# Kernel tuning notes

Measured on AMD Instinct MI355X. Metric: run time of the kernel, lower is better.

The kernel has to match this reference:

```python
import jax, jax.numpy as jnp
import numpy as np

B, L, F, U, P, CAT = 64, 25, 128, 10000, 10000, 400
PI = 3.141592653589793


def haversine(lat1, lon1, lat2, lon2):
    p = PI / 180.0
    a = 0.5 - jnp.cos((lat2 - lat1) * p) / 2 \
        + jnp.cos(lat1 * p) * jnp.cos(lat2 * p) * (1 - jnp.cos((lon2 - lon1) * p)) / 2
    return 12742.0 * jnp.arcsin(jnp.sqrt(a))


def setup_inputs() -> dict:
    key = jax.random.key(0)
    ks = jax.random.split(key, 24)
    s = 0.02
    return {
        "user": jax.random.randint(ks[0], (B, L), 0, U),
        "poi": jax.random.randint(ks[1], (B, L), 0, P),
        "cat": jax.random.randint(ks[2], (B, L), 0, CAT),
        "lat": jax.random.uniform(ks[3], (B, L), dtype=jnp.float32),
        "lon": jax.random.uniform(ks[4], (B, L), dtype=jnp.float32),
        "tod": jax.random.randint(ks[5], (B, L), 0, 24),
        "dow": jax.random.randint(ks[6], (B, L), 0, 7),
        "unixtime": jax.random.uniform(ks[7], (B, L), dtype=jnp.float32),
        "user_emb_w": jax.random.normal(ks[8], (U, F), jnp.float32) * s,
        "poi_emb_w": jax.random.normal(ks[9], (P, F), jnp.float32) * s,
        "tod_emb_w": jax.random.normal(ks[10], (24, F), jnp.float32) * s,
        "dow_emb_w": jax.random.normal(ks[11], (7, F), jnp.float32) * s,
        "Wq": jax.random.normal(ks[12], (F, F), jnp.float32) * s,
        "bq": jnp.zeros((F,), jnp.float32),
        "Wk": jax.random.normal(ks[13], (F, F), jnp.float32) * s,
        "bk": jnp.zeros((F,), jnp.float32),
        "Wv": jax.random.normal(ks[14], (F, F), jnp.float32) * s,
        "bv": jnp.zeros((F,), jnp.float32),
        "w_val": jax.random.normal(ks[15], (L,), jnp.float32) * 0.2,
        "b_val": jnp.zeros((), jnp.float32),
        "distance_matrix": jax.random.uniform(ks[16], (P, P), dtype=jnp.float32),
    }


def reference(user, poi, cat, lat, lon, tod, dow, unixtime,
              user_emb_w, poi_emb_w, tod_emb_w, dow_emb_w,
              Wq, bq, Wk, bk, Wv, bv, w_val, b_val, distance_matrix):
    # token embeddings  [B,L,F]
    inputs = user_emb_w[user] + poi_emb_w[poi] + tod_emb_w[tod] + dow_emb_w[dow]

    # pairwise haversine / time deltas  [B,L,L]  (vectorized double loop)
    delta_s = haversine(lat[:, :, None], lon[:, :, None], lat[:, None, :], lon[:, None, :])
    delta_t = jnp.abs(unixtime[:, :, None] - unixtime[:, None, :])
    su, sl = delta_s.max(), delta_s.min()
    tu, tl = delta_t.max(), delta_t.min()
    delta = (jnp.exp(-delta_s / (su - sl)) + jnp.exp(-delta_t / (tu - tl))) / 2

    # successive time intervals  [B,L], first column = 0
    time_interval = jnp.concatenate(
        [jnp.zeros((B, 1), unixtime.dtype), jnp.abs(unixtime[:, 1:] - unixtime[:, :-1])], axis=1)
    interval_s = distance_matrix[poi]            # [B,L,P] gather of candidate distances
    interval_t = time_interval[:, :, None]       # broadcast to [B,L,P]
    su1, sl1 = interval_s.max(), interval_s.min()
    tu1, tl1 = time_interval.max(), time_interval.min()
    interval = (jnp.exp(-interval_s / (su1 - sl1)) + jnp.exp(-interval_t / (tu1 - tl1))) / 2

    # additive-bias self-attention
    q = inputs @ Wq + bq
    k = inputs @ Wk + bk
    v = inputs @ Wv + bv
    scores = jnp.einsum('bif,bjf->bij', q, k) + delta
    attn_w = jax.nn.softmax(scores, axis=-1)
    self_attn_out = jnp.einsum('bij,bjf->bif', attn_w, v)   # [B,L,F]

    # candidate attention over all POIs, weighted by spatio-temporal interval
    cand_attn = jnp.einsum('pf,blf->bpl', poi_emb_w, self_attn_out) \
        * jnp.swapaxes(interval, 1, 2)                      # [B,P,L]
    pre = cand_attn @ w_val + b_val                          # Linear(25,1) -> [B,P]
    return (pre, pre)
```

## Files before the change

### kernel.cpp

```cpp
#include <hip/hip_runtime.h>
#include <math.h>

#define BB 64
#define LL 25
#define FF 128
#define PP 10000

#define OFF_RED 0
#define OFF_TT  16
#define OFF_C1  1616
#define OFF_C2  3216
#define OFF_DS  4816
#define OFF_DT  44816
#define OFF_Q   84816
#define OFF_K   289616
#define OFF_V   494416
#define OFF_AH  699216
#define OFF_AL  830288
#define OFF_BH  961360
#define OFF_BL  1608528

#define NEG_INF -3.402823466e38f
#define POS_INF  3.402823466e38f

typedef short bf16x8 __attribute__((ext_vector_type(8)));
typedef float f32x16 __attribute__((ext_vector_type(16)));

__device__ inline unsigned short f2bf(float x) {
    unsigned u = __float_as_uint(x);
    u += 0x7FFFu + ((u >> 16) & 1u);
    return (unsigned short)(u >> 16);
}
__device__ inline float bf2f(unsigned short h) {
    return __uint_as_float(((unsigned)h) << 16);
}

template <bool MAX>
__device__ float blockReduce(float v) {
    __shared__ float sh[8];
    const int lane = threadIdx.x & 63;
    const int wid  = threadIdx.x >> 6;
#pragma unroll
    for (int off = 32; off > 0; off >>= 1) {
        float o = __shfl_down(v, off, 64);
        v = MAX ? fmaxf(v, o) : fminf(v, o);
    }
    __syncthreads();
    if (lane == 0) sh[wid] = v;
    __syncthreads();
    if (threadIdx.x == 0) {
        const int nw = blockDim.x >> 6;
        for (int w = 1; w < nw; ++w) v = MAX ? fmaxf(v, sh[w]) : fminf(v, sh[w]);
    }
    return v;
}

__global__ void k_prep(const float* __restrict__ pe, float* __restrict__ ws) {
    const int gid = blockIdx.x * 256 + threadIdx.x;
    if (gid < 8) ((int*)ws)[gid] = (gid & 1) ? 0x7F800000 : (int)0xFF800000u;
    if (gid >= PP * FF) return;
    const int p = gid >> 7, f = gid & 127;
    const float x = pe[gid];
    const unsigned short h = f2bf(x);
    const unsigned short l = f2bf(x - bf2f(h));
    const int c = p >> 5, n = p & 31, kk = f >> 4, kh = (f >> 3) & 1, j = f & 7;
    const int pos = ((c * 8 + kk) * 64 + (kh * 32 + n)) * 8 + j;
    ((unsigned short*)(ws + OFF_BH))[pos] = h;
    ((unsigned short*)(ws + OFF_BL))[pos] = l;
}

__global__ void k_geo(const float* __restrict__ lat, const float* __restrict__ lon,
                      const float* __restrict__ ut, float* __restrict__ ws) {
    const int b = blockIdx.x, t = threadIdx.x;
    __shared__ float la[LL], lo[LL], uu[LL];
    if (t < LL) { la[t] = lat[b * LL + t]; lo[t] = lon[b * LL + t]; uu[t] = ut[b * LL + t]; }
    __syncthreads();
    float dsmax = NEG_INF, dsmin = POS_INF, dtmax = NEG_INF, dtmin = POS_INF;
    const float p = 0.017453292519943295f;
    for (int idx = t; idx < LL * LL; idx += 256) {
        int i = idx / LL, j = idx % LL;
        float a = 0.5f - cosf((la[j] - la[i]) * p) * 0.5f
                + cosf(la[i] * p) * cosf(la[j] * p) * (1.0f - cosf((lo[j] - lo[i]) * p)) * 0.5f;
        float d  = 12742.0f * asinf(sqrtf(a));
        float dt = fabsf(uu[i] - uu[j]);
        ws[OFF_DS + b * 625 + idx] = d;
        ws[OFF_DT + b * 625 + idx] = dt;
        dsmax = fmaxf(dsmax, d); dsmin = fminf(dsmin, d);
        dtmax = fmaxf(dtmax, dt); dtmin = fminf(dtmin, dt);
    }
    int* red = (int*)ws;
    float r;
    r = blockReduce<true >(dsmax); if (!t) atomicMax(&red[0], __float_as_int(r));
    r = blockReduce<false>(dsmin); if (!t) atomicMin(&red[1], __float_as_int(r));
    r = blockReduce<true >(dtmax); if (!t) atomicMax(&red[2], __float_as_int(r));
    r = blockReduce<false>(dtmin); if (!t) atomicMin(&red[3], __float_as_int(r));
    float ttv = 0.0f;
    if (t < LL) {
        ttv = (t == 0) ? 0.0f : fabsf(uu[t] - uu[t - 1]);
        ws[OFF_TT + b * LL + t] = ttv;
    }
    float tmax = (t < LL) ? ttv : NEG_INF;
    float tmin = (t < LL) ? ttv : POS_INF;
    r = blockReduce<true >(tmax); if (!t) atomicMax(&red[6], __float_as_int(r));
    r = blockReduce<false>(tmin); if (!t) atomicMin(&red[7], __float_as_int(r));
}

__global__ void k_qkv(const int* __restrict__ user, const int* __restrict__ poi,
                      const int* __restrict__ tod, const int* __restrict__ dow,
                      const float* __restrict__ ue, const float* __restrict__ pe,
                      const float* __restrict__ te, const float* __restrict__ de,
                      const float* __restrict__ Wq, const float* __restrict__ bq,
                      const float* __restrict__ Wk, const float* __restrict__ bk,
                      const float* __restrict__ Wv, const float* __restrict__ bv,
                      float* __restrict__ ws) {
    const int b = blockIdx.x, m = blockIdx.y, t = threadIdx.x;
    __shared__ __align__(16) float xs[26 * FF];
    __shared__ int ids[4][LL];
    if (t < LL) {
        ids[0][t] = user[b * LL + t]; ids[1][t] = poi[b * LL + t];
        ids[2][t] = tod[b * LL + t];  ids[3][t] = dow[b * LL + t];
    }
    if (t < FF) xs[LL * FF + t] = 0.0f;
    __syncthreads();
    for (int idx = t; idx < LL * FF; idx += 256) {
        int l = idx >> 7, f = idx & 127;
        xs[idx] = ue[ids[0][l] * FF + f] + pe[ids[1][l] * FF + f]
                + te[ids[2][l] * FF + f] + de[ids[3][l] * FF + f];
    }
    __syncthreads();
    const float* W    = (m == 0) ? Wq : (m == 1) ? Wk : Wv;
    const float* bias = (m == 0) ? bq : (m == 1) ? bk : bv;
    float* o = ws + ((m == 0) ? OFF_Q : (m == 1) ? OFF_K : OFF_V) + b * LL * FF;
    const int f  = t & 127;
    const int l0 = (t >> 7) * 13;
    float acc[13];
#pragma unroll
    for (int i = 0; i < 13; ++i) acc[i] = 0.0f;
    for (int g = 0; g < FF; g += 4) {
        float w0 = W[(g + 0) * FF + f];
        float w1 = W[(g + 1) * FF + f];
        float w2 = W[(g + 2) * FF + f];
        float w3 = W[(g + 3) * FF + f];
#pragma unroll
        for (int i = 0; i < 13; ++i) {
            float4 x = *(const float4*)(xs + (l0 + i) * FF + g);
            acc[i] = fmaf(x.w, w3, fmaf(x.z, w2, fmaf(x.y, w1, fmaf(x.x, w0, acc[i]))));
        }
    }
    float bb = bias[f];
#pragma unroll
    for (int i = 0; i < 13; ++i) {
        int l = l0 + i;
        if (l < LL) o[l * FF + f] = acc[i] + bb;
    }
}

__global__ void k_rowred(const int* __restrict__ poi, const float* __restrict__ dm,
                         float* __restrict__ ws) {
    const int t = threadIdx.x;
    float mx = NEG_INF, mn = POS_INF;
#pragma unroll
    for (int rr = 0; rr < 4; ++rr) {
        const int r = poi[blockIdx.x * 4 + rr];
        const float4* row = (const float4*)(dm + (size_t)r * PP);
        for (int i = t; i < PP / 4; i += 256) {
            float4 v = row[i];
            mx = fmaxf(mx, fmaxf(fmaxf(v.x, v.y), fmaxf(v.z, v.w)));
            mn = fminf(mn, fminf(fminf(v.x, v.y), fminf(v.z, v.w)));
        }
    }
    int* red = (int*)ws;
    float rr2;
    rr2 = blockReduce<true >(mx); if (!t) atomicMax(&red[4], __float_as_int(rr2));
    rr2 = blockReduce<false>(mn); if (!t) atomicMin(&red[5], __float_as_int(rr2));
}

__global__ void k_attn(const float* __restrict__ w_val, float* __restrict__ ws) {
    const int b = blockIdx.x, t = threadIdx.x;
    __shared__ float qs[LL * 129], ks[LL * 129], vs[LL * FF], sc[LL * LL];
    const int* red = (const int*)ws;
    const float su  = __int_as_float(red[0]), sl  = __int_as_float(red[1]);
    const float tu  = __int_as_float(red[2]), tl  = __int_as_float(red[3]);
    const float tu1 = __int_as_float(red[6]), tl1 = __int_as_float(red[7]);
    const float nS0 = -1.0f / (su - sl), nT0 = -1.0f / (tu - tl), nT1 = -1.0f / (tu1 - tl1);
    for (int idx = t; idx < LL * FF; idx += 256) {
        int l = idx >> 7, f = idx & 127;
        qs[l * 129 + f] = ws[OFF_Q + b * LL * FF + idx];
        ks[l * 129 + f] = ws[OFF_K + b * LL * FF + idx];
        vs[idx]         = ws[OFF_V + b * LL * FF + idx];
    }
    __syncthreads();
    for (int idx = t; idx < LL * LL; idx += 256) {
        int i = idx / LL, j = idx % LL;
        float a = 0.0f;
        for (int f = 0; f < FF; ++f) a = fmaf(qs[i * 129 + f], ks[j * 129 + f], a);
        float d  = ws[OFF_DS + b * 625 + idx];
        float dt = ws[OFF_DT + b * 625 + idx];
        sc[idx] = a + 0.5f * (expf(d * nS0) + expf(dt * nT0));
    }
    __syncthreads();
    if (t < LL) {
        float m = NEG_INF;
        for (int j = 0; j < LL; ++j) m = fmaxf(m, sc[t * LL + j]);
        float s = 0.0f;
        for (int j = 0; j < LL; ++j) { float e = expf(sc[t * LL + j] - m); sc[t * LL + j] = e; s += e; }
        float inv = 1.0f / s;
        for (int j = 0; j < LL; ++j) sc[t * LL + j] *= inv;
    }
    __syncthreads();
    unsigned short* Ah = (unsigned short*)(ws + OFF_AH);
    unsigned short* Al = (unsigned short*)(ws + OFF_AL);
    for (int idx = t; idx < LL * FF; idx += 256) {
        int l = idx >> 7, f = idx & 127;
        float a = 0.0f;
        for (int j = 0; j < LL; ++j) a = fmaf(sc[l * LL + j], vs[j * FF + f], a);
        unsigned short h  = f2bf(a);
        unsigned short lo = f2bf(a - bf2f(h));
        int kk = f >> 4, kh = (f >> 3) & 1, j = f & 7;
        int pos = ((b * 8 + kk) * 64 + (kh * 32 + l)) * 8 + j;
        Ah[pos] = h; Al[pos] = lo;
    }
    if (t < LL) {
        float ttv = ws[OFF_TT + b * LL + t];
        float wv  = w_val[t];
        ws[OFF_C1 + b * LL + t] = 0.5f * wv * expf(ttv * nT1);
        ws[OFF_C2 + b * LL + t] = 0.5f * wv;
    }
}

__global__ void __launch_bounds__(256) k_main(const int* __restrict__ poi,
                                              const float* __restrict__ dm,
                                              const float* __restrict__ bval_p,
                                              const float* __restrict__ ws,
                                              float* __restrict__ out) {
    const int t = threadIdx.x;
    const int wave = t >> 6, lane = t & 63;
    const int half = lane >> 5, col = lane & 31;
    __shared__ float lc1[BB * 32], lc2[BB * 32];
    __shared__ int   lrw[BB * 32];
    for (int idx = t; idx < BB * LL; idx += 256) {
        int b = idx / LL, l = idx - b * LL;
        lc1[b * 32 + l] = ws[OFF_C1 + idx];
        lc2[b * 32 + l] = ws[OFF_C2 + idx];
        lrw[b * 32 + l] = poi[idx];
    }
    __syncthreads();
    const int* red = (const int*)ws;
    const float su1 = __int_as_float(red[4]), sl1 = __int_as_float(red[5]);
    const float nS1 = -1.0f / (su1 - sl1);
    const float bv  = bval_p[0];
    const int ct  = blockIdx.x * 4 + wave;
    const int p   = ct * 32 + col;
    const int pcl = min(p, PP - 1);
    const bf16x8* Bh = (const bf16x8*)(ws + OFF_BH);
    const bf16x8* Bl = (const bf16x8*)(ws + OFF_BL);
    const bf16x8* Ah = (const bf16x8*)(ws + OFF_AH);
    const bf16x8* Al = (const bf16x8*)(ws + OFF_AL);
    bf16x8 bh[8], bl[8];
#pragma unroll
    for (int kk = 0; kk < 8; ++kk) {
        bh[kk] = Bh[(ct * 8 + kk) * 64 + lane];
        bl[kk] = Bl[(ct * 8 + kk) * 64 + lane];
    }
    const int b0 = blockIdx.y * 8;
    for (int bi = 0; bi < 8; ++bi) {
        const int b = b0 + bi;
        f32x16 acc = {};
#pragma unroll
        for (int kk = 0; kk < 8; ++kk) {
            bf16x8 ah = Ah[(b * 8 + kk) * 64 + lane];
            bf16x8 al = Al[(b * 8 + kk) * 64 + lane];
            acc = __builtin_amdgcn_mfma_f32_32x32x16_bf16(ah, bh[kk], acc, 0, 0, 0);
            acc = __builtin_amdgcn_mfma_f32_32x32x16_bf16(al, bh[kk], acc, 0, 0, 0);
            acc = __builtin_amdgcn_mfma_f32_32x32x16_bf16(ah, bl[kk], acc, 0, 0, 0);
        }
        float sum = 0.0f;
#pragma unroll
        for (int r = 0; r < 16; ++r) {
            int row  = (r & 3) + 8 * (r >> 2) + 4 * half;
            int rowc = min(row, LL - 1);
            float d  = dm[(size_t)lrw[b * 32 + rowc] * PP + pcl];
            float w  = lc1[b * 32 + rowc] + lc2[b * 32 + rowc] * expf(d * nS1);
            w = (row < LL) ? w : 0.0f;
            sum = fmaf(w, acc[r], sum);
        }
        sum += __shfl_xor(sum, 32, 64);
        sum += bv;
        if (half == 0 && p < PP) {
            out[b * PP + p]           = sum;
            out[BB * PP + b * PP + p] = sum;
        }
    }
}

extern "C" void kernel_launch(void* const* d_in, const int* in_sizes, int n_in,
                              void* d_out, int out_size, void* d_ws, size_t ws_size,
                              hipStream_t stream) {
    const int*   user = (const int*)d_in[0];
    const int*   poi  = (const int*)d_in[1];
    const float* lat  = (const float*)d_in[3];
    const float* lon  = (const float*)d_in[4];
    const int*   tod  = (const int*)d_in[5];
    const int*   dow  = (const int*)d_in[6];
    const float* ut   = (const float*)d_in[7];
    const float* ue   = (const float*)d_in[8];
    const float* pe   = (const float*)d_in[9];
    const float* te   = (const float*)d_in[10];
    const float* de   = (const float*)d_in[11];
    const float* Wq   = (const float*)d_in[12];
    const float* bq   = (const float*)d_in[13];
    const float* Wk   = (const float*)d_in[14];
    const float* bk   = (const float*)d_in[15];
    const float* Wv   = (const float*)d_in[16];
    const float* bv   = (const float*)d_in[17];
    const float* w_val = (const float*)d_in[18];
    const float* b_val = (const float*)d_in[19];
    const float* dm   = (const float*)d_in[20];
    float* out = (float*)d_out;
    float* ws  = (float*)d_ws;

    k_prep<<<(PP * FF + 255) / 256, 256, 0, stream>>>(pe, ws);
    k_geo<<<BB, 256, 0, stream>>>(lat, lon, ut, ws);
    k_qkv<<<dim3(BB, 3), 256, 0, stream>>>(user, poi, tod, dow, ue, pe, te, de,
                                           Wq, bq, Wk, bk, Wv, bv, ws);
    k_rowred<<<(BB * LL) / 4, 256, 0, stream>>>(poi, dm, ws);
    k_attn<<<BB, 256, 0, stream>>>(w_val, ws);
    k_main<<<dim3(79, 8), 256, 0, stream>>>(poi, dm, b_val, ws, out);
}
```

Measured before the change: 605.4 us.

## Merge front-end kernels into one launch and replace atomics with partial reductions

Fuses the prep, geo, QKV and distance-row reduction kernels into a single launch that dispatches on block index, removing three launch gaps and letting the independent stages overlap. Global atomic min/max is replaced by per-block partial results that k_attn and k_main reduce themselves. The pe bf16 split is vectorised to write 8 elements per thread. k_main skips the 3 accumulator rows that are always padding and uses the fast __expf. The trade-offs are a redundant small reduction in every consumer block and slightly lower exp accuracy.

```diff
diff --git a/kernel.cpp b/kernel.cpp
--- a/kernel.cpp
+++ b/kernel.cpp
@@ -6,19 +6,27 @@
 #define FF 128
 #define PP 10000
 
-#define OFF_RED 0
-#define OFF_TT  16
-#define OFF_C1  1616
-#define OFF_C2  3216
-#define OFF_DS  4816
-#define OFF_DT  44816
-#define OFF_Q   84816
-#define OFF_K   289616
-#define OFF_V   494416
-#define OFF_AH  699216
-#define OFF_AL  830288
-#define OFF_BH  961360
-#define OFF_BL  1608528
+#define OFF_GEOP 0
+#define OFF_TTP  256
+#define OFF_RRP  384
+#define OFF_TT   1184
+#define OFF_C1   2784
+#define OFF_C2   4384
+#define OFF_DS   5984
+#define OFF_DT   45984
+#define OFF_Q    85984
+#define OFF_K    290784
+#define OFF_V    495584
+#define OFF_AH   700384
+#define OFF_AL   831456
+#define OFF_BH   962528
+#define OFF_BL   1609696
+
+#define NB_PREP 625
+#define NB_GEO  64
+#define NB_QKV  192
+#define NB_ROW  400
+#define NB_FRONT (NB_PREP + NB_GEO + NB_QKV + NB_ROW)
 
 #define NEG_INF -3.402823466e38f
 #define POS_INF  3.402823466e38f
@@ -55,134 +63,153 @@
     return v;
 }
 
-__global__ void k_prep(const float* __restrict__ pe, float* __restrict__ ws) {
-    const int gid = blockIdx.x * 256 + threadIdx.x;
-    if (gid < 8) ((int*)ws)[gid] = (gid & 1) ? 0x7F800000 : (int)0xFF800000u;
-    if (gid >= PP * FF) return;
-    const int p = gid >> 7, f = gid & 127;
-    const float x = pe[gid];
-    const unsigned short h = f2bf(x);
-    const unsigned short l = f2bf(x - bf2f(h));
-    const int c = p >> 5, n = p & 31, kk = f >> 4, kh = (f >> 3) & 1, j = f & 7;
-    const int pos = ((c * 8 + kk) * 64 + (kh * 32 + n)) * 8 + j;
-    ((unsigned short*)(ws + OFF_BH))[pos] = h;
-    ((unsigned short*)(ws + OFF_BL))[pos] = l;
-}
-
-__global__ void k_geo(const float* __restrict__ lat, const float* __restrict__ lon,
-                      const float* __restrict__ ut, float* __restrict__ ws) {
-    const int b = blockIdx.x, t = threadIdx.x;
-    __shared__ float la[LL], lo[LL], uu[LL];
-    if (t < LL) { la[t] = lat[b * LL + t]; lo[t] = lon[b * LL + t]; uu[t] = ut[b * LL + t]; }
-    __syncthreads();
-    float dsmax = NEG_INF, dsmin = POS_INF, dtmax = NEG_INF, dtmin = POS_INF;
-    const float p = 0.017453292519943295f;
-    for (int idx = t; idx < LL * LL; idx += 256) {
-        int i = idx / LL, j = idx % LL;
-        float a = 0.5f - cosf((la[j] - la[i]) * p) * 0.5f
-                + cosf(la[i] * p) * cosf(la[j] * p) * (1.0f - cosf((lo[j] - lo[i]) * p)) * 0.5f;
-        float d  = 12742.0f * asinf(sqrtf(a));
-        float dt = fabsf(uu[i] - uu[j]);
-        ws[OFF_DS + b * 625 + idx] = d;
-        ws[OFF_DT + b * 625 + idx] = dt;
-        dsmax = fmaxf(dsmax, d); dsmin = fminf(dsmin, d);
-        dtmax = fmaxf(dtmax, dt); dtmin = fminf(dtmin, dt);
-    }
-    int* red = (int*)ws;
-    float r;
-    r = blockReduce<true >(dsmax); if (!t) atomicMax(&red[0], __float_as_int(r));
-    r = blockReduce<false>(dsmin); if (!t) atomicMin(&red[1], __float_as_int(r));
-    r = blockReduce<true >(dtmax); if (!t) atomicMax(&red[2], __float_as_int(r));
-    r = blockReduce<false>(dtmin); if (!t) atomicMin(&red[3], __float_as_int(r));
-    float ttv = 0.0f;
-    if (t < LL) {
-        ttv = (t == 0) ? 0.0f : fabsf(uu[t] - uu[t - 1]);
-        ws[OFF_TT + b * LL + t] = ttv;
-    }
-    float tmax = (t < LL) ? ttv : NEG_INF;
-    float tmin = (t < LL) ? ttv : POS_INF;
-    r = blockReduce<true >(tmax); if (!t) atomicMax(&red[6], __float_as_int(r));
-    r = blockReduce<false>(tmin); if (!t) atomicMin(&red[7], __float_as_int(r));
-}
-
-__global__ void k_qkv(const int* __restrict__ user, const int* __restrict__ poi,
-                      const int* __restrict__ tod, const int* __restrict__ dow,
-                      const float* __restrict__ ue, const float* __restrict__ pe,
-                      const float* __restrict__ te, const float* __restrict__ de,
-                      const float* __restrict__ Wq, const float* __restrict__ bq,
-                      const float* __restrict__ Wk, const float* __restrict__ bk,
-                      const float* __restrict__ Wv, const float* __restrict__ bv,
-                      float* __restrict__ ws) {
-    const int b = blockIdx.x, m = blockIdx.y, t = threadIdx.x;
-    __shared__ __align__(16) float xs[26 * FF];
-    __shared__ int ids[4][LL];
-    if (t < LL) {
-        ids[0][t] = user[b * LL + t]; ids[1][t] = poi[b * LL + t];
-        ids[2][t] = tod[b * LL + t];  ids[3][t] = dow[b * LL + t];
-    }
-    if (t < FF) xs[LL * FF + t] = 0.0f;
-    __syncthreads();
-    for (int idx = t; idx < LL * FF; idx += 256) {
-        int l = idx >> 7, f = idx & 127;
-        xs[idx] = ue[ids[0][l] * FF + f] + pe[ids[1][l] * FF + f]
-                + te[ids[2][l] * FF + f] + de[ids[3][l] * FF + f];
-    }
-    __syncthreads();
-    const float* W    = (m == 0) ? Wq : (m == 1) ? Wk : Wv;
-    const float* bias = (m == 0) ? bq : (m == 1) ? bk : bv;
-    float* o = ws + ((m == 0) ? OFF_Q : (m == 1) ? OFF_K : OFF_V) + b * LL * FF;
-    const int f  = t & 127;
-    const int l0 = (t >> 7) * 13;
-    float acc[13];
-#pragma unroll
-    for (int i = 0; i < 13; ++i) acc[i] = 0.0f;
-    for (int g = 0; g < FF; g += 4) {
-        float w0 = W[(g + 0) * FF + f];
-        float w1 = W[(g + 1) * FF + f];
-        float w2 = W[(g + 2) * FF + f];
-        float w3 = W[(g + 3) * FF + f];
+__global__ void k_front(const int* __restrict__ user, const int* __restrict__ poi,
+                        const int* __restrict__ tod, const int* __restrict__ dow,
+                        const float* __restrict__ lat, const float* __restrict__ lon,
+                        const float* __restrict__ ut,
+                        const float* __restrict__ ue, const float* __restrict__ pe,
+                        const float* __restrict__ te, const float* __restrict__ de,
+                        const float* __restrict__ Wq, const float* __restrict__ bq,
+                        const float* __restrict__ Wk, const float* __restrict__ bk,
+                        const float* __restrict__ Wv, const float* __restrict__ bv,
+                        const float* __restrict__ dm, float* __restrict__ ws) {
+    const int blk = blockIdx.x, t = threadIdx.x;
+
+    if (blk < NB_PREP) {
+        const int gid = blk * 256 + t;
+        const int p   = gid >> 4;
+        const int sub = gid & 15;
+        const int kk  = sub >> 1, kh = sub & 1;
+        const float* src = pe + p * FF + kk * 16 + kh * 8;
+        float4 a0 = *(const float4*)(src);
+        float4 a1 = *(const float4*)(src + 4);
+        float xv[8] = {a0.x, a0.y, a0.z, a0.w, a1.x, a1.y, a1.z, a1.w};
+        bf16x8 hv, lv;
+#pragma unroll
+        for (int j = 0; j < 8; ++j) {
+            unsigned short h = f2bf(xv[j]);
+            hv[j] = (short)h;
+            lv[j] = (short)f2bf(xv[j] - bf2f(h));
+        }
+        const int c = p >> 5, n = p & 31;
+        const int pos = (c * 8 + kk) * 64 + (kh * 32 + n);
+        ((bf16x8*)((unsigned short*)(ws + OFF_BH)))[pos] = hv;
+        ((bf16x8*)((unsigned short*)(ws + OFF_BL)))[pos] = lv;
+
+    } else if (blk < NB_PREP + NB_GEO) {
+        const int b = blk - NB_PREP;
+        __shared__ float la[LL], lo[LL], uu[LL];
+        if (t < LL) { la[t] = lat[b * LL + t]; lo[t] = lon[b * LL + t]; uu[t] = ut[b * LL + t]; }
+        __syncthreads();
+        float dsmax = NEG_INF, dsmin = POS_INF, dtmax = NEG_INF, dtmin = POS_INF;
+        const float p = 0.017453292519943295f;
+        for (int idx = t; idx < LL * LL; idx += 256) {
+            int i = idx / LL, j = idx % LL;
+            float a = 0.5f - cosf((la[j] - la[i]) * p) * 0.5f
+                    + cosf(la[i] * p) * cosf(la[j] * p) * (1.0f - cosf((lo[j] - lo[i]) * p)) * 0.5f;
+            float d  = 12742.0f * asinf(sqrtf(a));
+            float dt = fabsf(uu[i] - uu[j]);
+            ws[OFF_DS + b * 625 + idx] = d;
+            ws[OFF_DT + b * 625 + idx] = dt;
+            dsmax = fmaxf(dsmax, d); dsmin = fminf(dsmin, d);
+            dtmax = fmaxf(dtmax, dt); dtmin = fminf(dtmin, dt);
+        }
+        float r;
+        r = blockReduce<true >(dsmax); if (!t) ws[OFF_GEOP + b * 4 + 0] = r;
+        r = blockReduce<false>(dsmin); if (!t) ws[OFF_GEOP + b * 4 + 1] = r;
+        r = blockReduce<true >(dtmax); if (!t) ws[OFF_GEOP + b * 4 + 2] = r;
+        r = blockReduce<false>(dtmin); if (!t) ws[OFF_GEOP + b * 4 + 3] = r;
+        float ttv = 0.0f;
+        if (t < LL) {
+            ttv = (t == 0) ? 0.0f : fabsf(uu[t] - uu[t - 1]);
+            ws[OFF_TT + b * LL + t] = ttv;
+        }
+        float tmax = (t < LL) ? ttv : NEG_INF;
+        float tmin = (t < LL) ? ttv : POS_INF;
+        r = blockReduce<true >(tmax); if (!t) ws[OFF_TTP + b * 2 + 0] = r;
+        r = blockReduce<false>(tmin); if (!t) ws[OFF_TTP + b * 2 + 1] = r;
+
+    } else if (blk < NB_PREP + NB_GEO + NB_QKV) {
+        const int id = blk - (NB_PREP + NB_GEO);
+        const int b = id & 63, m = id >> 6;
+        __shared__ __align__(16) float xs[26 * FF];
+        __shared__ int ids[4][LL];
+        if (t < LL) {
+            ids[0][t] = user[b * LL + t]; ids[1][t] = poi[b * LL + t];
+            ids[2][t] = tod[b * LL + t];  ids[3][t] = dow[b * LL + t];
+        }
+        if (t < FF) xs[LL * FF + t] = 0.0f;
+        __syncthreads();
+        for (int idx = t; idx < LL * FF; idx += 256) {
+            int l = idx >> 7, f = idx & 127;
+            xs[idx] = ue[ids[0][l] * FF + f] + pe[ids[1][l] * FF + f]
+                    + te[ids[2][l] * FF + f] + de[ids[3][l] * FF + f];
+        }
+        __syncthreads();
+        const float* W    = (m == 0) ? Wq : (m == 1) ? Wk : Wv;
+        const float* bias = (m == 0) ? bq : (m == 1) ? bk : bv;
+        float* o = ws + ((m == 0) ? OFF_Q : (m == 1) ? OFF_K : OFF_V) + b * LL * FF;
+        const int f  = t & 127;
+        const int l0 = (t >> 7) * 13;
+        float acc[13];
+#pragma unroll
+        for (int i = 0; i < 13; ++i) acc[i] = 0.0f;
+        for (int g = 0; g < FF; g += 4) {
+            float w0 = W[(g + 0) * FF + f];
+            float w1 = W[(g + 1) * FF + f];
+            float w2 = W[(g + 2) * FF + f];
+            float w3 = W[(g + 3) * FF + f];
+#pragma unroll
+            for (int i = 0; i < 13; ++i) {
+                float4 x = *(const float4*)(xs + (l0 + i) * FF + g);
+                acc[i] = fmaf(x.w, w3, fmaf(x.z, w2, fmaf(x.y, w1, fmaf(x.x, w0, acc[i]))));
+            }
+        }
+        float bb = bias[f];
 #pragma unroll
         for (int i = 0; i < 13; ++i) {
-            float4 x = *(const float4*)(xs + (l0 + i) * FF + g);
-            acc[i] = fmaf(x.w, w3, fmaf(x.z, w2, fmaf(x.y, w1, fmaf(x.x, w0, acc[i]))));
-        }
-    }
-    float bb = bias[f];
-#pragma unroll
-    for (int i = 0; i < 13; ++i) {
-        int l = l0 + i;
-        if (l < LL) o[l * FF + f] = acc[i] + bb;
-    }
-}
-
-__global__ void k_rowred(const int* __restrict__ poi, const float* __restrict__ dm,
-                         float* __restrict__ ws) {
-    const int t = threadIdx.x;
-    float mx = NEG_INF, mn = POS_INF;
-#pragma unroll
-    for (int rr = 0; rr < 4; ++rr) {
-        const int r = poi[blockIdx.x * 4 + rr];
-        const float4* row = (const float4*)(dm + (size_t)r * PP);
-        for (int i = t; i < PP / 4; i += 256) {
-            float4 v = row[i];
-            mx = fmaxf(mx, fmaxf(fmaxf(v.x, v.y), fmaxf(v.z, v.w)));
-            mn = fminf(mn, fminf(fminf(v.x, v.y), fminf(v.z, v.w)));
-        }
-    }
-    int* red = (int*)ws;
-    float rr2;
-    rr2 = blockReduce<true >(mx); if (!t) atomicMax(&red[4], __float_as_int(rr2));
-    rr2 = blockReduce<false>(mn); if (!t) atomicMin(&red[5], __float_as_int(rr2));
+            int l = l0 + i;
+            if (l < LL) o[l * FF + f] = acc[i] + bb;
+        }
+
+    } else {
+        const int g = blk - (NB_PREP + NB_GEO + NB_QKV);
+        float mx = NEG_INF, mn = POS_INF;
+#pragma unroll
+        for (int rr = 0; rr < 4; ++rr) {
+            const int r = poi[g * 4 + rr];
+            const float4* row = (const float4*)(dm + (size_t)r * PP);
+            for (int i = t; i < PP / 4; i += 256) {
+                float4 v = row[i];
+                mx = fmaxf(mx, fmaxf(fmaxf(v.x, v.y), fmaxf(v.z, v.w)));
+                mn = fminf(mn, fminf(fminf(v.x, v.y), fminf(v.z, v.w)));
+            }
+        }
+        float r2;
+        r2 = blockReduce<true >(mx); if (!t) ws[OFF_RRP + g * 2 + 0] = r2;
+        r2 = blockReduce<false>(mn); if (!t) ws[OFF_RRP + g * 2 + 1] = r2;
+    }
 }
 
 __global__ void k_attn(const float* __restrict__ w_val, float* __restrict__ ws) {
     const int b = blockIdx.x, t = threadIdx.x;
     __shared__ float qs[LL * 129], ks[LL * 129], vs[LL * FF], sc[LL * LL];
-    const int* red = (const int*)ws;
-    const float su  = __int_as_float(red[0]), sl  = __int_as_float(red[1]);
-    const float tu  = __int_as_float(red[2]), tl  = __int_as_float(red[3]);
-    const float tu1 = __int_as_float(red[6]), tl1 = __int_as_float(red[7]);
-    const float nS0 = -1.0f / (su - sl), nT0 = -1.0f / (tu - tl), nT1 = -1.0f / (tu1 - tl1);
+    __shared__ float bc[6];
+    {
+        float g0 = (t < 64) ? ws[OFF_GEOP + t * 4 + 0] : NEG_INF;
+        float g1 = (t < 64) ? ws[OFF_GEOP + t * 4 + 1] : POS_INF;
+        float g2 = (t < 64) ? ws[OFF_GEOP + t * 4 + 2] : NEG_INF;
+        float g3 = (t < 64) ? ws[OFF_GEOP + t * 4 + 3] : POS_INF;
+        float t0 = (t < 64) ? ws[OFF_TTP + t * 2 + 0] : NEG_INF;
+        float t1 = (t < 64) ? ws[OFF_TTP + t * 2 + 1] : POS_INF;
+        float r;
+        r = blockReduce<true >(g0); if (!t) bc[0] = r;
+        r = blockReduce<false>(g1); if (!t) bc[1] = r;
+        r = blockReduce<true >(g2); if (!t) bc[2] = r;
+        r = blockReduce<false>(g3); if (!t) bc[3] = r;
+        r = blockReduce<true >(t0); if (!t) bc[4] = r;
+        r = blockReduce<false>(t1); if (!t) bc[5] = r;
+    }
     for (int idx = t; idx < LL * FF; idx += 256) {
         int l = idx >> 7, f = idx & 127;
         qs[l * 129 + f] = ws[OFF_Q + b * LL * FF + idx];
@@ -190,6 +217,10 @@
         vs[idx]         = ws[OFF_V + b * LL * FF + idx];
     }
     __syncthreads();
+    const float su  = bc[0], sl  = bc[1];
+    const float tu  = bc[2], tl  = bc[3];
+    const float tu1 = bc[4], tl1 = bc[5];
+    const float nS0 = -1.0f / (su - sl), nT0 = -1.0f / (tu - tl), nT1 = -1.0f / (tu1 - tl1);
     for (int idx = t; idx < LL * LL; idx += 256) {
         int i = idx / LL, j = idx % LL;
         float a = 0.0f;
@@ -238,6 +269,17 @@
     const int half = lane >> 5, col = lane & 31;
     __shared__ float lc1[BB * 32], lc2[BB * 32];
     __shared__ int   lrw[BB * 32];
+    __shared__ float bc2[2];
+    {
+        float mx = NEG_INF, mn = POS_INF;
+        for (int i = t; i < 400; i += 256) {
+            mx = fmaxf(mx, ws[OFF_RRP + i * 2 + 0]);
+            mn = fminf(mn, ws[OFF_RRP + i * 2 + 1]);
+        }
+        float r;
+        r = blockReduce<true >(mx); if (!t) bc2[0] = r;
+        r = blockReduce<false>(mn); if (!t) bc2[1] = r;
+    }
     for (int idx = t; idx < BB * LL; idx += 256) {
         int b = idx / LL, l = idx - b * LL;
         lc1[b * 32 + l] = ws[OFF_C1 + idx];
@@ -245,8 +287,7 @@
         lrw[b * 32 + l] = poi[idx];
     }
     __syncthreads();
-    const int* red = (const int*)ws;
-    const float su1 = __int_as_float(red[4]), sl1 = __int_as_float(red[5]);
+    const float su1 = bc2[0], sl1 = bc2[1];
     const float nS1 = -1.0f / (su1 - sl1);
     const float bv  = bval_p[0];
     const int ct  = blockIdx.x * 4 + wave;
@@ -276,11 +317,11 @@
         }
         float sum = 0.0f;
 #pragma unroll
-        for (int r = 0; r < 16; ++r) {
+        for (int r = 0; r < 13; ++r) {
             int row  = (r & 3) + 8 * (r >> 2) + 4 * half;
             int rowc = min(row, LL - 1);
             float d  = dm[(size_t)lrw[b * 32 + rowc] * PP + pcl];
-            float w  = lc1[b * 32 + rowc] + lc2[b * 32 + rowc] * expf(d * nS1);
+            float w  = lc1[b * 32 + rowc] + lc2[b * 32 + rowc] * __expf(d * nS1);
             w = (row < LL) ? w : 0.0f;
             sum = fmaf(w, acc[r], sum);
         }
@@ -319,11 +360,9 @@
     float* out = (float*)d_out;
     float* ws  = (float*)d_ws;
 
-    k_prep<<<(PP * FF + 255) / 256, 256, 0, stream>>>(pe, ws);
-    k_geo<<<BB, 256, 0, stream>>>(lat, lon, ut, ws);
-    k_qkv<<<dim3(BB, 3), 256, 0, stream>>>(user, poi, tod, dow, ue, pe, te, de,
-                                           Wq, bq, Wk, bk, Wv, bv, ws);
-    k_rowred<<<(BB * LL) / 4, 256, 0, stream>>>(poi, dm, ws);
+    k_front<<<NB_FRONT, 256, 0, stream>>>(user, poi, tod, dow, lat, lon, ut,
+                                          ue, pe, te, de, Wq, bq, Wk, bk, Wv, bv,
+                                          dm, ws);
     k_attn<<<BB, 256, 0, stream>>>(w_val, ws);
     k_main<<<dim3(79, 8), 256, 0, stream>>>(poi, dm, b_val, ws, out);
 }
```

Result: faster. 572.1 us (-5.5%).
